# Performance work log

Hardware: AMD Instinct MI355X
Metric: run time of the kernel (lower is better)

The kernel has to match this reference:

```python
import jax, jax.numpy as jnp
import numpy as np

DIM = 256
HEADS = 4
B, N = 2, 4096
NEG = -1e9
EPS = 1e-5


def setup_inputs() -> dict:
    key = jax.random.key(0)
    ks = jax.random.split(key, 12)
    s = 0.02
    inp = {
        "x": jax.random.normal(ks[0], (B, N, DIM), dtype=jnp.float32),
        "adj": jax.random.randint(ks[1], (B, N, N), 0, 2, dtype=jnp.int32),
        "Wq": jax.random.normal(ks[2], (DIM, DIM), dtype=jnp.float32) * s,
        "bq": jnp.zeros((DIM,), jnp.float32),
        "Wk": jax.random.normal(ks[3], (DIM, DIM), dtype=jnp.float32) * s,
        "bk": jnp.zeros((DIM,), jnp.float32),
        "Wv": jax.random.normal(ks[4], (DIM, DIM), dtype=jnp.float32) * s,
        "bv": jnp.zeros((DIM,), jnp.float32),
        "Wo": jax.random.normal(ks[5], (DIM, DIM), dtype=jnp.float32) * s,
        "bo": jnp.zeros((DIM,), jnp.float32),
        "gamma": jnp.ones((DIM,), jnp.float32),
        "beta": jnp.zeros((DIM,), jnp.float32),
    }
    return inp


def reference(x, adj, Wq, bq, Wk, bk, Wv, bv, Wo, bo, gamma, beta):
    Bx, Nx, C = x.shape
    H = HEADS
    D = C // H
    scale = D ** (-0.5)
    # torch Linear: y = x @ W.T + b
    def proj(W, b):
        return (x @ W.T + b).reshape(Bx, Nx, H, D).transpose(0, 2, 1, 3)  # [B,H,N,D]
    q = proj(Wq, bq)
    k = proj(Wk, bk)
    v = proj(Wv, bv)
    attn = jnp.einsum("bhnd,bhmd->bhnm", q, k) * scale          # [B,H,N,N]
    attn = jnp.where(adj[:, None, :, :] == 0, NEG, attn)
    attn = jax.nn.softmax(attn, axis=-1)
    # dropout omitted (eval mode / deterministic reference)
    out = jnp.einsum("bhnm,bhmd->bhnd", attn, v)                # [B,H,N,D]
    out = out.transpose(0, 2, 1, 3).reshape(Bx, Nx, C)
    out = out @ Wo.T + bo
    mu = jnp.mean(out, axis=-1, keepdims=True)
    var = jnp.var(out, axis=-1, keepdims=True)
    return (out - mu) * jax.lax.rsqrt(var + EPS) * gamma + beta
```

## Files before the change

### kernel.cpp

```cpp
#include <hip/hip_runtime.h>
#include <stdint.h>

#define CDIM 256
#define HEADS 4
#define HD 64
#define NB 2
#define NN 4096

typedef unsigned short u16;
typedef unsigned char u8;
typedef unsigned long long u64;
typedef __attribute__((ext_vector_type(8))) short short8;
typedef __attribute__((ext_vector_type(4))) float f32x4;

#define QSCALE 0.1803368801111244f

__device__ __forceinline__ u16 f2bf(float f) {
  union { float f; unsigned u; } v; v.f = f;
  return (u16)((v.u + 0x7fffu + ((v.u >> 16) & 1u)) >> 16);
}
__device__ __forceinline__ float bf2f(u16 u) {
  union { unsigned u; float f; } v; v.u = ((unsigned)u) << 16; return v.f;
}
__device__ __forceinline__ short8 fragf32(const float* p) {
  float4 a = reinterpret_cast<const float4*>(p)[0];
  float4 b = reinterpret_cast<const float4*>(p)[1];
  short8 h;
  h[0] = (short)f2bf(a.x); h[1] = (short)f2bf(a.y);
  h[2] = (short)f2bf(a.z); h[3] = (short)f2bf(a.w);
  h[4] = (short)f2bf(b.x); h[5] = (short)f2bf(b.y);
  h[6] = (short)f2bf(b.z); h[7] = (short)f2bf(b.w);
  return h;
}

__global__ __launch_bounds__(256) void prep(
    const int* __restrict__ adj, u8* __restrict__ bmb,
    const float* __restrict__ Wq, const float* __restrict__ Wk,
    const float* __restrict__ Wv, const float* __restrict__ Wo,
    u16* __restrict__ Wqb, u16* __restrict__ Wkb,
    u16* __restrict__ Wvb, u16* __restrict__ Wob) {
  const int blk = blockIdx.x;
  if (blk < 4096) {
    const int wave = threadIdx.x >> 6, lane = threadIdx.x & 63;
    const int c0 = blk * 16 + wave * 4;
#pragma unroll
    for (int it = 0; it < 4; ++it) {
      int c = c0 + it;
      int row = c >> 3, kb = (c & 7) * 512;
      const int* src = adj + (size_t)row * 4096 + kb + lane * 8;
      uint4 a = *reinterpret_cast<const uint4*>(src);
      uint4 b = *reinterpret_cast<const uint4*>(src + 4);
      unsigned byte = 0;
      byte |= (a.x != 0) ? 1u : 0u;
      byte |= (a.y != 0) ? 2u : 0u;
      byte |= (a.z != 0) ? 4u : 0u;
      byte |= (a.w != 0) ? 8u : 0u;
      byte |= (b.x != 0) ? 16u : 0u;
      byte |= (b.y != 0) ? 32u : 0u;
      byte |= (b.z != 0) ? 64u : 0u;
      byte |= (b.w != 0) ? 128u : 0u;
      bmb[(size_t)row * 512 + (c & 7) * 64 + lane] = (u8)byte;
    }
  } else {
    size_t base = ((size_t)(blk - 4096) * 256 + threadIdx.x) * 8;
    int w = (int)(base >> 16);
    size_t lo = base & 65535;
    const float* src;
    u16* dst;
    if (w == 0)      { src = Wq + lo; dst = Wqb + lo; }
    else if (w == 1) { src = Wk + lo; dst = Wkb + lo; }
    else if (w == 2) { src = Wv + lo; dst = Wvb + lo; }
    else             { src = Wo + lo; dst = Wob + lo; }
    *reinterpret_cast<short8*>(dst) = fragf32(src);
  }
}

__global__ __launch_bounds__(256) void qkv_gemm(
    const float* __restrict__ x,
    const u16* __restrict__ Wqb, const u16* __restrict__ Wkb,
    const u16* __restrict__ Wvb,
    const float* __restrict__ bq, const float* __restrict__ bk,
    const float* __restrict__ bv,
    u16* __restrict__ Qb, u16* __restrict__ Kb, u16* __restrict__ Vtb) {
  const int tid = threadIdx.x, w = tid >> 6, lane = tid & 63;
  const int quad = lane >> 4, l15 = lane & 15;
  const int tok0 = blockIdx.x * 16;
  const int b = tok0 >> 12, nl = tok0 & 4095;
  const int ym = blockIdx.y;

  f32x4 acc[4];
#pragma unroll
  for (int i = 0; i < 4; ++i) acc[i] = (f32x4){0.f, 0.f, 0.f, 0.f};

  if (ym < 2) {
    const u16* Wb = (ym == 0) ? Wqb : Wkb;
    const float* bias = (ym == 0) ? bq : bk;
    const float scale = (ym == 0) ? QSCALE : 1.0f;
    u16* outp = (ym == 0) ? Qb : Kb;
#pragma unroll
    for (int ks = 0; ks < 8; ++ks) {
      short8 af = fragf32(x + (size_t)(tok0 + l15) * 256 + ks * 32 + quad * 8);
#pragma unroll
      for (int ns = 0; ns < 4; ++ns) {
        short8 bf = *reinterpret_cast<const short8*>(
            &Wb[(size_t)(w * 64 + ns * 16 + l15) * 256 + ks * 32 + quad * 8]);
        acc[ns] = __builtin_amdgcn_mfma_f32_16x16x32_bf16(af, bf, acc[ns], 0, 0, 0);
      }
    }
#pragma unroll
    for (int ns = 0; ns < 4; ++ns) {
      int d = ns * 16 + l15;
      float bb = bias[w * 64 + d];
#pragma unroll
      for (int r = 0; r < 4; ++r) {
        int tok = nl + quad * 4 + r;
        outp[((size_t)(b * HEADS + w) * NN + tok) * HD + d] =
            f2bf((acc[ns][r] + bb) * scale);
      }
    }
  } else {
#pragma unroll
    for (int ks = 0; ks < 8; ++ks) {
      short8 xf = fragf32(x + (size_t)(tok0 + l15) * 256 + ks * 32 + quad * 8);
#pragma unroll
      for (int ms = 0; ms < 4; ++ms) {
        short8 wf = *reinterpret_cast<const short8*>(
            &Wvb[(size_t)(w * 64 + ms * 16 + l15) * 256 + ks * 32 + quad * 8]);
        acc[ms] = __builtin_amdgcn_mfma_f32_16x16x32_bf16(wf, xf, acc[ms], 0, 0, 0);
      }
    }
#pragma unroll
    for (int ms = 0; ms < 4; ++ms) {
#pragma unroll
      for (int r = 0; r < 4; ++r) {
        int d = ms * 16 + quad * 4 + r;
        float bb = bv[w * 64 + d];
        Vtb[((size_t)((b * HEADS + w) * HD + d)) * NN + nl + l15] =
            f2bf(acc[ms][r] + bb);
      }
    }
  }
}

__global__ __launch_bounds__(256) void attn_mfma(
    const u16* __restrict__ Qb, const u16* __restrict__ Kb,
    const u16* __restrict__ Vtb, const u64* __restrict__ bm,
    u16* __restrict__ Opb, float* __restrict__ Lp) {
  __shared__ u16 Ks[64 * 72];
  __shared__ u16 Vs[64 * 72];
  __shared__ u16 Ps[4][16 * 72];

  const int tid = threadIdx.x;
  const int wave = tid >> 6, lane = tid & 63;
  const int quad = lane >> 4, l15 = lane & 15;
  const int bh = blockIdx.y, b = bh >> 2, h = bh & 3;
  const int q0 = blockIdx.x * 64 + wave * 16;
  const int half = blockIdx.z;
  const int key0 = half * 2048;

  const u16* qr = Qb + ((size_t)bh * NN + q0 + l15) * HD + quad * 8;
  const short8 qf0 = *reinterpret_cast<const short8*>(qr);
  const short8 qf1 = *reinterpret_cast<const short8*>(qr + 32);

  short8 ones;
#pragma unroll
  for (int i = 0; i < 8; ++i) ones[i] = (short)0x3F80;

  f32x4 Oacc[4];
#pragma unroll
  for (int i = 0; i < 4; ++i) Oacc[i] = (f32x4){0.f, 0.f, 0.f, 0.f};
  f32x4 Oli = (f32x4){0.f, 0.f, 0.f, 0.f};
  const f32x4 z4 = {0.f, 0.f, 0.f, 0.f};
  u16* Pw = &Ps[wave][0];
  const u64* bmr = bm + ((size_t)b * NN + q0 + quad * 4) * 64 + half * 32;

  const u16* kbase = Kb + (size_t)bh * NN * HD;
  const u16* vbase = Vtb + (size_t)bh * HD * NN;
  const int rr = tid >> 3, cc8 = (tid & 7) * 8;
  const int rr2 = rr + 32;

  uint4 k0, k1, v0, v1;
  k0 = *reinterpret_cast<const uint4*>(kbase + (size_t)(key0 + rr) * HD + cc8);
  k1 = *reinterpret_cast<const uint4*>(kbase + (size_t)(key0 + rr2) * HD + cc8);
  v0 = *reinterpret_cast<const uint4*>(vbase + (size_t)rr * NN + key0 + cc8);
  v1 = *reinterpret_cast<const uint4*>(vbase + (size_t)rr2 * NN + key0 + cc8);

  for (int mt = 0; mt < 32; ++mt) {
    __syncthreads();
    *reinterpret_cast<uint4*>(&Ks[rr * 72 + cc8]) = k0;
    *reinterpret_cast<uint4*>(&Ks[rr2 * 72 + cc8]) = k1;
    *reinterpret_cast<uint4*>(&Vs[rr * 72 + cc8]) = v0;
    *reinterpret_cast<uint4*>(&Vs[rr2 * 72 + cc8]) = v1;
    __syncthreads();
    if (mt + 1 < 32) {
      int kb2 = key0 + (mt + 1) * 64;
      k0 = *reinterpret_cast<const uint4*>(kbase + (size_t)(kb2 + rr) * HD + cc8);
      k1 = *reinterpret_cast<const uint4*>(kbase + (size_t)(kb2 + rr2) * HD + cc8);
      v0 = *reinterpret_cast<const uint4*>(vbase + (size_t)rr * NN + kb2 + cc8);
      v1 = *reinterpret_cast<const uint4*>(vbase + (size_t)rr2 * NN + kb2 + cc8);
    }

    u64 am[4];
#pragma unroll
    for (int r = 0; r < 4; ++r) am[r] = bmr[r * 64 + mt];

#pragma unroll
    for (int t = 0; t < 4; ++t) {
      const u16* kr = &Ks[(t * 16 + l15) * 72 + quad * 8];
      short8 kf0 = *reinterpret_cast<const short8*>(kr);
      short8 kf1 = *reinterpret_cast<const short8*>(kr + 32);
      f32x4 s = __builtin_amdgcn_mfma_f32_16x16x32_bf16(qf0, kf0, z4, 0, 0, 0);
      s = __builtin_amdgcn_mfma_f32_16x16x32_bf16(qf1, kf1, s, 0, 0, 0);
      const int sh = t * 16 + l15;
      float pr[4];
#pragma unroll
      for (int r = 0; r < 4; ++r)
        pr[r] = ((unsigned)(am[r] >> sh) & 1u) ? exp2f(s[r]) : 0.f;
      unsigned pk[4];
#pragma unroll
      for (int r = 0; r < 4; ++r) {
        unsigned pv = __float_as_uint(pr[r]);
        unsigned nb = __float_as_uint(__shfl_xor(pr[r], 1, 64));
        pk[r] = (pv >> 16) | (nb & 0xffff0000u);
      }
      if ((l15 & 1) == 0) {
#pragma unroll
        for (int r = 0; r < 4; ++r)
          *reinterpret_cast<unsigned*>(&Pw[(quad * 4 + r) * 72 + sh]) = pk[r];
      }
    }
    __asm__ volatile("s_waitcnt lgkmcnt(0)" ::: "memory");

    const short8 pf0 = *reinterpret_cast<const short8*>(&Pw[l15 * 72 + quad * 8]);
    const short8 pf1 = *reinterpret_cast<const short8*>(&Pw[l15 * 72 + 32 + quad * 8]);
    Oli = __builtin_amdgcn_mfma_f32_16x16x32_bf16(pf0, ones, Oli, 0, 0, 0);
    Oli = __builtin_amdgcn_mfma_f32_16x16x32_bf16(pf1, ones, Oli, 0, 0, 0);
#pragma unroll
    for (int dt = 0; dt < 4; ++dt) {
      const u16* vr = &Vs[(dt * 16 + l15) * 72 + quad * 8];
      short8 vf0 = *reinterpret_cast<const short8*>(vr);
      short8 vf1 = *reinterpret_cast<const short8*>(vr + 32);
      Oacc[dt] = __builtin_amdgcn_mfma_f32_16x16x32_bf16(pf0, vf0, Oacc[dt], 0, 0, 0);
      Oacc[dt] = __builtin_amdgcn_mfma_f32_16x16x32_bf16(pf1, vf1, Oacc[dt], 0, 0, 0);
    }
  }

  u16* ob = Opb + (size_t)(half * NB + b) * NN * CDIM;
#pragma unroll
  for (int r = 0; r < 4; ++r) {
    int tok = q0 + quad * 4 + r;
    if (l15 == 0) Lp[((size_t)half * 8 + bh) * NN + tok] = Oli[r];
#pragma unroll
    for (int dt = 0; dt < 4; ++dt)
      ob[(size_t)tok * CDIM + h * HD + dt * 16 + l15] = f2bf(Oacc[dt][r]);
  }
}

__global__ __launch_bounds__(256) void comb_oproj(
    const u16* __restrict__ Opb, const float* __restrict__ Lp,
    const u16* __restrict__ Wob, const float* __restrict__ bo,
    const float* __restrict__ gamma, const float* __restrict__ beta,
    float* __restrict__ out) {
  __shared__ u16 As[16 * 264];
  __shared__ float ys[16][264];
  __shared__ float linv[64];
  const int tid = threadIdx.x, w = tid >> 6, lane = tid & 63;
  const int quad = lane >> 4, l15 = lane & 15;
  const int tok0 = blockIdx.x * 16;
  const int b = tok0 >> 12, nl = tok0 & 4095;

  if (tid < 64) {
    int tokr = tid >> 2, hh = tid & 3;
    int bh = b * 4 + hh;
    int n = nl + tokr;
    float s = Lp[(size_t)bh * NN + n] + Lp[(size_t)(8 + bh) * NN + n];
    linv[tokr * 4 + hh] = (s > 0.f) ? (1.f / s) : 0.f;
  }
  __syncthreads();

  {
    int tokr = tid >> 4, ch0 = (tid & 15) * 16;
    size_t base = ((size_t)b * NN + nl + tokr) * CDIM + ch0;
    uint4 a0 = *reinterpret_cast<const uint4*>(Opb + base);
    uint4 a1 = *reinterpret_cast<const uint4*>(Opb + base + 8);
    uint4 c0 = *reinterpret_cast<const uint4*>(Opb + 2097152 + base);
    uint4 c1 = *reinterpret_cast<const uint4*>(Opb + 2097152 + base + 8);
    float inv = linv[tokr * 4 + (ch0 >> 6)];
    unsigned wa[8] = {a0.x, a0.y, a0.z, a0.w, a1.x, a1.y, a1.z, a1.w};
    unsigned wb[8] = {c0.x, c0.y, c0.z, c0.w, c1.x, c1.y, c1.z, c1.w};
    u16 ov[16];
#pragma unroll
    for (int i = 0; i < 8; ++i) {
      float lo = (bf2f((u16)(wa[i] & 0xffffu)) + bf2f((u16)(wb[i] & 0xffffu))) * inv;
      float hi = (bf2f((u16)(wa[i] >> 16)) + bf2f((u16)(wb[i] >> 16))) * inv;
      ov[2 * i] = f2bf(lo);
      ov[2 * i + 1] = f2bf(hi);
    }
    u16* dst = &As[tokr * 264 + ch0];
    *reinterpret_cast<uint4*>(dst) = *reinterpret_cast<uint4*>(ov);
    *reinterpret_cast<uint4*>(dst + 8) = *reinterpret_cast<uint4*>(ov + 8);
  }
  __syncthreads();

  f32x4 acc[4];
#pragma unroll
  for (int i = 0; i < 4; ++i) acc[i] = (f32x4){0.f, 0.f, 0.f, 0.f};
#pragma unroll
  for (int ks = 0; ks < 8; ++ks) {
    short8 af = *reinterpret_cast<const short8*>(&As[l15 * 264 + ks * 32 + quad * 8]);
#pragma unroll
    for (int ns = 0; ns < 4; ++ns) {
      short8 bf = *reinterpret_cast<const short8*>(
          &Wob[(size_t)(w * 64 + ns * 16 + l15) * 256 + ks * 32 + quad * 8]);
      acc[ns] = __builtin_amdgcn_mfma_f32_16x16x32_bf16(af, bf, acc[ns], 0, 0, 0);
    }
  }

#pragma unroll
  for (int ns = 0; ns < 4; ++ns) {
    int ch = w * 64 + ns * 16 + l15;
    float bb = bo[ch];
#pragma unroll
    for (int r = 0; r < 4; ++r) ys[quad * 4 + r][ch] = acc[ns][r] + bb;
  }
  __syncthreads();

  float g[4], bt[4];
#pragma unroll
  for (int i = 0; i < 4; ++i) {
    g[i] = gamma[lane + i * 64];
    bt[i] = beta[lane + i * 64];
  }
#pragma unroll
  for (int rr = 0; rr < 4; ++rr) {
    int r = w * 4 + rr;
    float v[4], s = 0.f, s2 = 0.f;
#pragma unroll
    for (int i = 0; i < 4; ++i) {
      v[i] = ys[r][lane + i * 64];
      s += v[i];
      s2 = fmaf(v[i], v[i], s2);
    }
#pragma unroll
    for (int off = 32; off > 0; off >>= 1) {
      s += __shfl_xor(s, off, 64);
      s2 += __shfl_xor(s2, off, 64);
    }
    float mu = s * (1.f / 256.f);
    float rs = rsqrtf(s2 * (1.f / 256.f) - mu * mu + 1e-5f);
    float* orow = out + (size_t)(tok0 + r) * 256;
#pragma unroll
    for (int i = 0; i < 4; ++i)
      orow[lane + i * 64] = (v[i] - mu) * rs * g[i] + bt[i];
  }
}

extern "C" void kernel_launch(void* const* d_in, const int* in_sizes, int n_in,
                              void* d_out, int out_size, void* d_ws, size_t ws_size,
                              hipStream_t stream) {
  const float* x     = (const float*)d_in[0];
  const int*   adj   = (const int*)d_in[1];
  const float* Wq    = (const float*)d_in[2];
  const float* bq    = (const float*)d_in[3];
  const float* Wk    = (const float*)d_in[4];
  const float* bk    = (const float*)d_in[5];
  const float* Wv    = (const float*)d_in[6];
  const float* bv    = (const float*)d_in[7];
  const float* Wo    = (const float*)d_in[8];
  const float* bo    = (const float*)d_in[9];
  const float* gamma = (const float*)d_in[10];
  const float* beta  = (const float*)d_in[11];
  float* out = (float*)d_out;

  const size_t PER = (size_t)NB * HEADS * NN * HD;
  u16* Wqb = (u16*)d_ws;
  u16* Wkb = Wqb + 65536;
  u16* Wvb = Wkb + 65536;
  u16* Wob = Wvb + 65536;
  u64* bmp = (u64*)(Wob + 65536);
  u16* Qb  = (u16*)(bmp + 524288);
  u16* Kb  = Qb + PER;
  u16* Vtb = Kb + PER;
  u16* Opb = Vtb + PER;
  float* Lp = (float*)(Opb + 2 * PER);

  const size_t NEED = (size_t)((u16*)(Lp + 65536) - (u16*)d_ws) * sizeof(u16);
  if (ws_size < NEED) return;

  prep<<<dim3(4224), dim3(256), 0, stream>>>(
      adj, (u8*)bmp, Wq, Wk, Wv, Wo, Wqb, Wkb, Wvb, Wob);

  qkv_gemm<<<dim3(512, 3), dim3(256), 0, stream>>>(
      x, Wqb, Wkb, Wvb, bq, bk, bv, Qb, Kb, Vtb);

  attn_mfma<<<dim3(NN / 64, NB * HEADS, 2), dim3(256), 0, stream>>>(
      Qb, Kb, Vtb, bmp, Opb, Lp);

  comb_oproj<<<dim3((NB * NN) / 16), dim3(256), 0, stream>>>(
      Opb, Lp, Wob, bo, gamma, beta, out);
}
```

Baseline: 353.6 us.

## Rewrite attention core with 32x32 MFMA, in-register P, double-buffered swizzled LDS

```diff
diff --git a/kernel.cpp b/kernel.cpp
--- a/kernel.cpp
+++ b/kernel.cpp
@@ -12,6 +12,7 @@
 typedef unsigned long long u64;
 typedef __attribute__((ext_vector_type(8))) short short8;
 typedef __attribute__((ext_vector_type(4))) float f32x4;
+typedef __attribute__((ext_vector_type(16))) float f32x16;
 
 #define QSCALE 0.1803368801111244f
 
@@ -31,6 +32,20 @@
   h[4] = (short)f2bf(b.x); h[5] = (short)f2bf(b.y);
   h[6] = (short)f2bf(b.z); h[7] = (short)f2bf(b.w);
   return h;
+}
+__device__ __forceinline__ f32x16 zero16() {
+  f32x16 z;
+#pragma unroll
+  for (int i = 0; i < 16; ++i) z[i] = 0.f;
+  return z;
+}
+__device__ __forceinline__ unsigned cvt_pk_bf16(float lo, float hi) {
+  unsigned r;
+  asm("v_cvt_pk_bf16_f32 %0, %1, %2" : "=v"(r) : "v"(lo), "v"(hi));
+  return r;
+}
+__device__ __forceinline__ void permlane32_swap(unsigned& a, unsigned& b) {
+  asm("v_permlane32_swap_b32 %0, %1" : "+v"(a), "+v"(b));
 }
 
 __global__ __launch_bounds__(256) void prep(
@@ -146,113 +161,155 @@
     const u16* __restrict__ Qb, const u16* __restrict__ Kb,
     const u16* __restrict__ Vtb, const u64* __restrict__ bm,
     u16* __restrict__ Opb, float* __restrict__ Lp) {
-  __shared__ u16 Ks[64 * 72];
-  __shared__ u16 Vs[64 * 72];
-  __shared__ u16 Ps[4][16 * 72];
+  __shared__ __align__(16) u16 KVs[2 * 8192];
 
   const int tid = threadIdx.x;
   const int wave = tid >> 6, lane = tid & 63;
-  const int quad = lane >> 4, l15 = lane & 15;
+  const int h5 = lane >> 5, l31 = lane & 31, l7 = lane & 7;
   const int bh = blockIdx.y, b = bh >> 2, h = bh & 3;
-  const int q0 = blockIdx.x * 64 + wave * 16;
+  const int q0 = blockIdx.x * 128 + wave * 32;
   const int half = blockIdx.z;
   const int key0 = half * 2048;
 
-  const u16* qr = Qb + ((size_t)bh * NN + q0 + l15) * HD + quad * 8;
+  const u16* qr = Qb + ((size_t)bh * NN + q0 + l31) * HD + h5 * 8;
   const short8 qf0 = *reinterpret_cast<const short8*>(qr);
-  const short8 qf1 = *reinterpret_cast<const short8*>(qr + 32);
+  const short8 qf1 = *reinterpret_cast<const short8*>(qr + 16);
+  const short8 qf2 = *reinterpret_cast<const short8*>(qr + 32);
+  const short8 qf3 = *reinterpret_cast<const short8*>(qr + 48);
 
   short8 ones;
 #pragma unroll
   for (int i = 0; i < 8; ++i) ones[i] = (short)0x3F80;
 
-  f32x4 Oacc[4];
-#pragma unroll
-  for (int i = 0; i < 4; ++i) Oacc[i] = (f32x4){0.f, 0.f, 0.f, 0.f};
-  f32x4 Oli = (f32x4){0.f, 0.f, 0.f, 0.f};
-  const f32x4 z4 = {0.f, 0.f, 0.f, 0.f};
-  u16* Pw = &Ps[wave][0];
-  const u64* bmr = bm + ((size_t)b * NN + q0 + quad * 4) * 64 + half * 32;
-
-  const u16* kbase = Kb + (size_t)bh * NN * HD;
-  const u16* vbase = Vtb + (size_t)bh * HD * NN;
-  const int rr = tid >> 3, cc8 = (tid & 7) * 8;
-  const int rr2 = rr + 32;
+  f32x16 Oacc0 = zero16(), Oacc1 = zero16(), Oli = zero16();
+
+  int sdk[4];
+#pragma unroll
+  for (int j = 0; j < 4; ++j) sdk[j] = ((2 * j + h5) ^ l7) << 3;
+
+  const int srow = tid >> 2;
+  const int wbu0 = ((((tid & 3) * 2)     ^ (srow & 7)) << 3) + srow * 64;
+  const int wbu1 = ((((tid & 3) * 2 + 1) ^ (srow & 7)) << 3) + srow * 64;
+
+  const u16* kbase = Kb + (size_t)bh * NN * HD + (size_t)key0 * HD;
+  const u16* vbase = Vtb + (size_t)bh * HD * NN + key0;
+  const u64* bmr = bm + ((size_t)b * NN + q0 + l31) * 64 + half * 32;
 
   uint4 k0, k1, v0, v1;
-  k0 = *reinterpret_cast<const uint4*>(kbase + (size_t)(key0 + rr) * HD + cc8);
-  k1 = *reinterpret_cast<const uint4*>(kbase + (size_t)(key0 + rr2) * HD + cc8);
-  v0 = *reinterpret_cast<const uint4*>(vbase + (size_t)rr * NN + key0 + cc8);
-  v1 = *reinterpret_cast<const uint4*>(vbase + (size_t)rr2 * NN + key0 + cc8);
+  {
+    const uint4* kp = reinterpret_cast<const uint4*>(kbase) + tid * 2;
+    k0 = kp[0]; k1 = kp[1];
+    const u16* vp = vbase + (size_t)srow * NN + (tid & 3) * 16;
+    v0 = *reinterpret_cast<const uint4*>(vp);
+    v1 = *reinterpret_cast<const uint4*>(vp + 8);
+  }
+  *reinterpret_cast<uint4*>(&KVs[wbu0]) = k0;
+  *reinterpret_cast<uint4*>(&KVs[wbu1]) = k1;
+  *reinterpret_cast<uint4*>(&KVs[4096 + wbu0]) = v0;
+  *reinterpret_cast<uint4*>(&KVs[4096 + wbu1]) = v1;
+  {
+    const uint4* kp = reinterpret_cast<const uint4*>(kbase + 4096) + tid * 2;
+    k0 = kp[0]; k1 = kp[1];
+    const u16* vp = vbase + (size_t)srow * NN + 64 + (tid & 3) * 16;
+    v0 = *reinterpret_cast<const uint4*>(vp);
+    v1 = *reinterpret_cast<const uint4*>(vp + 8);
+  }
+  u64 amc = bmr[0];
 
   for (int mt = 0; mt < 32; ++mt) {
     __syncthreads();
-    *reinterpret_cast<uint4*>(&Ks[rr * 72 + cc8]) = k0;
-    *reinterpret_cast<uint4*>(&Ks[rr2 * 72 + cc8]) = k1;
-    *reinterpret_cast<uint4*>(&Vs[rr * 72 + cc8]) = v0;
-    *reinterpret_cast<uint4*>(&Vs[rr2 * 72 + cc8]) = v1;
-    __syncthreads();
+    const u64 am = amc;
+    if (mt + 1 < 32) amc = bmr[mt + 1];
+    const int cb = (mt & 1) * 8192;
+
+    f32x16 s0 = zero16(), s1 = zero16();
+#pragma unroll
+    for (int dk = 0; dk < 4; ++dk) {
+      short8 a0 = *reinterpret_cast<const short8*>(&KVs[cb + l31 * 64 + sdk[dk]]);
+      short8 a1 = *reinterpret_cast<const short8*>(&KVs[cb + 2048 + l31 * 64 + sdk[dk]]);
+      const short8 qf = (dk == 0) ? qf0 : (dk == 1) ? qf1 : (dk == 2) ? qf2 : qf3;
+      s0 = __builtin_amdgcn_mfma_f32_32x32x16_bf16(a0, qf, s0, 0, 0, 0);
+      s1 = __builtin_amdgcn_mfma_f32_32x32x16_bf16(a1, qf, s1, 0, 0, 0);
+    }
+
+    const u64 ash = am >> (4 * h5);
+    const unsigned mlo = (unsigned)ash, mhi = (unsigned)(ash >> 32);
+
+    uint4 pf0, pf1, pf2, pf3;
+    {
+      float pp[16];
+#pragma unroll
+      for (int r = 0; r < 16; ++r) {
+        const int c = (r & 3) + 8 * (r >> 2);
+        pp[r] = ((mlo >> c) & 1u) ? __builtin_amdgcn_exp2f(s0[r]) : 0.f;
+      }
+      unsigned wAe = cvt_pk_bf16(pp[0], pp[1]),  wBe = cvt_pk_bf16(pp[2], pp[3]);
+      unsigned wAo = cvt_pk_bf16(pp[4], pp[5]),  wBo = cvt_pk_bf16(pp[6], pp[7]);
+      permlane32_swap(wAe, wAo);
+      permlane32_swap(wBe, wBo);
+      pf0 = (uint4){wAe, wBe, wAo, wBo};
+      wAe = cvt_pk_bf16(pp[8], pp[9]);   wBe = cvt_pk_bf16(pp[10], pp[11]);
+      wAo = cvt_pk_bf16(pp[12], pp[13]); wBo = cvt_pk_bf16(pp[14], pp[15]);
+      permlane32_swap(wAe, wAo);
+      permlane32_swap(wBe, wBo);
+      pf1 = (uint4){wAe, wBe, wAo, wBo};
+    }
+    {
+      float pp[16];
+#pragma unroll
+      for (int r = 0; r < 16; ++r) {
+        const int c = (r & 3) + 8 * (r >> 2);
+        pp[r] = ((mhi >> c) & 1u) ? __builtin_amdgcn_exp2f(s1[r]) : 0.f;
+      }
+      unsigned wAe = cvt_pk_bf16(pp[0], pp[1]),  wBe = cvt_pk_bf16(pp[2], pp[3]);
+      unsigned wAo = cvt_pk_bf16(pp[4], pp[5]),  wBo = cvt_pk_bf16(pp[6], pp[7]);
+      permlane32_swap(wAe, wAo);
+      permlane32_swap(wBe, wBo);
+      pf2 = (uint4){wAe, wBe, wAo, wBo};
+      wAe = cvt_pk_bf16(pp[8], pp[9]);   wBe = cvt_pk_bf16(pp[10], pp[11]);
+      wAo = cvt_pk_bf16(pp[12], pp[13]); wBo = cvt_pk_bf16(pp[14], pp[15]);
+      permlane32_swap(wAe, wAo);
+      permlane32_swap(wBe, wBo);
+      pf3 = (uint4){wAe, wBe, wAo, wBo};
+    }
+
+#pragma unroll
+    for (int kb = 0; kb < 4; ++kb) {
+      union { uint4 u; short8 s; } cv;
+      cv.u = (kb == 0) ? pf0 : (kb == 1) ? pf1 : (kb == 2) ? pf2 : pf3;
+      const short8 pa = cv.s;
+      Oli = __builtin_amdgcn_mfma_f32_32x32x16_bf16(pa, ones, Oli, 0, 0, 0);
+      short8 vf0 = *reinterpret_cast<const short8*>(&KVs[cb + 4096 + l31 * 64 + sdk[kb]]);
+      short8 vf1 = *reinterpret_cast<const short8*>(&KVs[cb + 6144 + l31 * 64 + sdk[kb]]);
+      Oacc0 = __builtin_amdgcn_mfma_f32_32x32x16_bf16(pa, vf0, Oacc0, 0, 0, 0);
+      Oacc1 = __builtin_amdgcn_mfma_f32_32x32x16_bf16(pa, vf1, Oacc1, 0, 0, 0);
+    }
+
     if (mt + 1 < 32) {
-      int kb2 = key0 + (mt + 1) * 64;
-      k0 = *reinterpret_cast<const uint4*>(kbase + (size_t)(kb2 + rr) * HD + cc8);
-      k1 = *reinterpret_cast<const uint4*>(kbase + (size_t)(kb2 + rr2) * HD + cc8);
-      v0 = *reinterpret_cast<const uint4*>(vbase + (size_t)rr * NN + kb2 + cc8);
-      v1 = *reinterpret_cast<const uint4*>(vbase + (size_t)rr2 * NN + kb2 + cc8);
-    }
-
-    u64 am[4];
-#pragma unroll
-    for (int r = 0; r < 4; ++r) am[r] = bmr[r * 64 + mt];
-
-#pragma unroll
-    for (int t = 0; t < 4; ++t) {
-      const u16* kr = &Ks[(t * 16 + l15) * 72 + quad * 8];
-      short8 kf0 = *reinterpret_cast<const short8*>(kr);
-      short8 kf1 = *reinterpret_cast<const short8*>(kr + 32);
-      f32x4 s = __builtin_amdgcn_mfma_f32_16x16x32_bf16(qf0, kf0, z4, 0, 0, 0);
-      s = __builtin_amdgcn_mfma_f32_16x16x32_bf16(qf1, kf1, s, 0, 0, 0);
-      const int sh = t * 16 + l15;
-      float pr[4];
-#pragma unroll
-      for (int r = 0; r < 4; ++r)
-        pr[r] = ((unsigned)(am[r] >> sh) & 1u) ? exp2f(s[r]) : 0.f;
-      unsigned pk[4];
-#pragma unroll
-      for (int r = 0; r < 4; ++r) {
-        unsigned pv = __float_as_uint(pr[r]);
-        unsigned nb = __float_as_uint(__shfl_xor(pr[r], 1, 64));
-        pk[r] = (pv >> 16) | (nb & 0xffff0000u);
-      }
-      if ((l15 & 1) == 0) {
-#pragma unroll
-        for (int r = 0; r < 4; ++r)
-          *reinterpret_cast<unsigned*>(&Pw[(quad * 4 + r) * 72 + sh]) = pk[r];
-      }
-    }
-    __asm__ volatile("s_waitcnt lgkmcnt(0)" ::: "memory");
-
-    const short8 pf0 = *reinterpret_cast<const short8*>(&Pw[l15 * 72 + quad * 8]);
-    const short8 pf1 = *reinterpret_cast<const short8*>(&Pw[l15 * 72 + 32 + quad * 8]);
-    Oli = __builtin_amdgcn_mfma_f32_16x16x32_bf16(pf0, ones, Oli, 0, 0, 0);
-    Oli = __builtin_amdgcn_mfma_f32_16x16x32_bf16(pf1, ones, Oli, 0, 0, 0);
-#pragma unroll
-    for (int dt = 0; dt < 4; ++dt) {
-      const u16* vr = &Vs[(dt * 16 + l15) * 72 + quad * 8];
-      short8 vf0 = *reinterpret_cast<const short8*>(vr);
-      short8 vf1 = *reinterpret_cast<const short8*>(vr + 32);
-      Oacc[dt] = __builtin_amdgcn_mfma_f32_16x16x32_bf16(pf0, vf0, Oacc[dt], 0, 0, 0);
-      Oacc[dt] = __builtin_amdgcn_mfma_f32_16x16x32_bf16(pf1, vf1, Oacc[dt], 0, 0, 0);
+      const int nb = ((mt + 1) & 1) * 8192;
+      *reinterpret_cast<uint4*>(&KVs[nb + wbu0]) = k0;
+      *reinterpret_cast<uint4*>(&KVs[nb + wbu1]) = k1;
+      *reinterpret_cast<uint4*>(&KVs[nb + 4096 + wbu0]) = v0;
+      *reinterpret_cast<uint4*>(&KVs[nb + 4096 + wbu1]) = v1;
+      if (mt + 2 < 32) {
+        const uint4* kp =
+            reinterpret_cast<const uint4*>(kbase + (size_t)(mt + 2) * 4096) + tid * 2;
+        k0 = kp[0]; k1 = kp[1];
+        const u16* vp = vbase + (size_t)srow * NN + (mt + 2) * 64 + (tid & 3) * 16;
+        v0 = *reinterpret_cast<const uint4*>(vp);
+        v1 = *reinterpret_cast<const uint4*>(vp + 8);
+      }
     }
   }
 
   u16* ob = Opb + (size_t)(half * NB + b) * NN * CDIM;
 #pragma unroll
-  for (int r = 0; r < 4; ++r) {
-    int tok = q0 + quad * 4 + r;
-    if (l15 == 0) Lp[((size_t)half * 8 + bh) * NN + tok] = Oli[r];
-#pragma unroll
-    for (int dt = 0; dt < 4; ++dt)
-      ob[(size_t)tok * CDIM + h * HD + dt * 16 + l15] = f2bf(Oacc[dt][r]);
+  for (int r = 0; r < 16; ++r) {
+    const int tok = q0 + (r & 3) + 8 * (r >> 2) + 4 * h5;
+    u16* orow = ob + (size_t)tok * CDIM + h * HD;
+    orow[l31] = f2bf(Oacc0[r]);
+    orow[32 + l31] = f2bf(Oacc1[r]);
+    if (l31 == 0) Lp[((size_t)half * 8 + bh) * NN + tok] = Oli[r];
   }
 }
 
@@ -393,7 +450,7 @@
   qkv_gemm<<<dim3(512, 3), dim3(256), 0, stream>>>(
       x, Wqb, Wkb, Wvb, bq, bk, bv, Qb, Kb, Vtb);
 
-  attn_mfma<<<dim3(NN / 64, NB * HEADS, 2), dim3(256), 0, stream>>>(
+  attn_mfma<<<dim3(NN / 128, NB * HEADS, 2), dim3(256), 0, stream>>>(
       Qb, Kb, Vtb, bmp, Opb, Lp);
 
   comb_oproj<<<dim3((NB * NN) / 16), dim3(256), 0, stream>>>(
```

After: 317.7 us. -10.1%, faster.
